# Kernel optimization log

Measured on AMD Instinct MI355X. Metric: run time of the kernel, lower is better.

Reference implementation:

```python
import jax, jax.numpy as jnp
import numpy as np

B, S, D, H, L, E, FF = 16, 1024, 384, 8, 3, 8, 768
DH = D // H
TOP_K = 2


def _ln(x, s, b):
    m = x.mean(-1, keepdims=True)
    v = x.var(-1, keepdims=True)
    return (x - m) * jax.lax.rsqrt(v + 1e-5) * s + b


def setup_inputs() -> dict:
    key = jax.random.key(0)
    ks = jax.random.split(key, 12)
    def n(k, shp, scale=0.02):
        return jax.random.normal(k, shp, jnp.float32) * scale
    return dict(
        x=jax.random.normal(ks[0], (B, S, 1), jnp.float32),
        proj_w=n(ks[1], (1, D)), proj_b=jnp.zeros((D,), jnp.float32),
        qkv_w=n(ks[2], (L, D, 3 * D)), qkv_b=jnp.zeros((L, 3 * D), jnp.float32),
        out_w=n(ks[3], (L, D, D)), out_b=jnp.zeros((L, D), jnp.float32),
        n1_s=jnp.ones((L, D), jnp.float32), n1_b=jnp.zeros((L, D), jnp.float32),
        n2_s=jnp.ones((L, D), jnp.float32), n2_b=jnp.zeros((L, D), jnp.float32),
        gate_w=n(ks[4], (L, D, E)),
        e_w1=n(ks[5], (L, E, D, FF)), e_b1=jnp.zeros((L, E, FF), jnp.float32),
        e_w2=n(ks[6], (L, E, FF, D)), e_b2=jnp.zeros((L, E, D), jnp.float32),
        att_w=n(ks[7], (D,)), att_b=jnp.zeros((), jnp.float32),
        head_w=n(ks[8], (D, 1)), head_b=jnp.zeros((1,), jnp.float32),
    )


def reference(x, proj_w, proj_b, qkv_w, qkv_b, out_w, out_b,
              n1_s, n1_b, n2_s, n2_b, gate_w, e_w1, e_b1, e_w2, e_b2,
              att_w, att_b, head_w, head_b):
    # feature projection: [B,S,1] -> [B,S,D]
    h = x @ proj_w + proj_b
    total_moe = jnp.zeros((), h.dtype)
    scale = np.float32(1.0 / np.sqrt(DH))
    for l in range(L):
        # --- pre-norm multi-head self-attention ---
        xn = _ln(h, n1_s[l], n1_b[l])
        qkv = xn @ qkv_w[l] + qkv_b[l]
        q, k, v = jnp.split(qkv, 3, axis=-1)
        q = q.reshape(B, S, H, DH)
        k = k.reshape(B, S, H, DH)
        v = v.reshape(B, S, H, DH)
        attn = jax.nn.softmax(jnp.einsum('bqhd,bkhd->bhqk', q, k) * scale, axis=-1)
        ao = jnp.einsum('bhqk,bkhd->bqhd', attn, v).reshape(B, S, D)
        h = h + (ao @ out_w[l] + out_b[l])
        # --- pre-norm top-2 gated MoE FFN ---
        xn2 = _ln(h, n2_s[l], n2_b[l])
        probs = jax.nn.softmax(xn2 @ gate_w[l], axis=-1)            # [B,S,E]
        topv, topi = jax.lax.top_k(probs, TOP_K)
        gates = topv / topv.sum(-1, keepdims=True)                  # renormalized top-2
        full = (jax.nn.one_hot(topi, E, dtype=h.dtype) * gates[..., None]).sum(-2)  # [B,S,E]
        moe_out = jnp.zeros_like(h)
        for e in range(E):  # fixed small expert loop
            ye = jax.nn.relu(xn2 @ e_w1[l, e] + e_b1[l, e]) @ e_w2[l, e] + e_b2[l, e]
            moe_out = moe_out + full[..., e:e + 1] * ye
        h = h + moe_out
        # switch-style load-balancing aux loss
        importance = probs.reshape(-1, E).mean(0)
        load = (full > 0).astype(h.dtype).reshape(-1, E).mean(0)
        total_moe = total_moe + E * jnp.sum(importance * load)
    w = jax.nn.softmax(h @ att_w + att_b, axis=1)                   # [B,S]
    pooled = jnp.einsum('bs,bsd->bd', w, h)
    rul = pooled @ head_w + head_b                                  # [B,1]
    return rul, total_moe
```

## Files before the change

### kernel.cpp

```cpp
#include <hip/hip_runtime.h>
#include <hip/hip_bf16.h>
#include <math.h>

#define TOKENS 16384
#define DMODEL 384
#define SEQ 1024
#define NHEAD 8
#define DHEAD 48
#define NEXP 8
#define FFDIM 768
#define NL 3

typedef __bf16 bf16x8 __attribute__((ext_vector_type(8)));
typedef __bf16 bf16x4 __attribute__((ext_vector_type(4)));
typedef float f32x4 __attribute__((ext_vector_type(4)));

__global__ void finalize_kernel(const int* __restrict__ counts_all,
                                const float* __restrict__ sp_all, float* __restrict__ out) {
  float tm = 0.f;
  for (int l = 0; l < NL; l++) {
    float t = 0.f;
    for (int e = 0; e < NEXP; e++)
      t += sp_all[l * NEXP + e] * (float)counts_all[l * NEXP + e];
    tm += (float)NEXP * t / ((float)TOKENS * (float)TOKENS);
  }
  out[16] = tm;
}

__global__ __launch_bounds__(256) void proj_kernel(const float* __restrict__ x,
    const float* __restrict__ pw, const float* __restrict__ pb, float* __restrict__ h) {
  int i = blockIdx.x * 256 + threadIdx.x;
  int t = i / DMODEL;
  int d = i - t * DMODEL;
  h[i] = x[t] * pw[d] + pb[d];
}

__global__ __launch_bounds__(256) void convw_kernel(const float* __restrict__ src,
    __bf16* __restrict__ dst, int K, int N) {
  __shared__ float t[32][33];
  size_t boff = (size_t)blockIdx.z * K * N;
  src += boff; dst += boff;
  int k0 = blockIdx.y * 32, n0 = blockIdx.x * 32;
  int tx = threadIdx.x & 31, ty = threadIdx.x >> 5;
#pragma unroll
  for (int i = 0; i < 32; i += 8) t[ty + i][tx] = src[(size_t)(k0 + ty + i) * N + n0 + tx];
  __syncthreads();
#pragma unroll
  for (int i = 0; i < 32; i += 8)
    dst[(size_t)(n0 + ty + i) * K + k0 + tx] = (__bf16)t[tx][ty + i];
}

__global__ __launch_bounds__(384) void ln_kernel(const float* __restrict__ src,
    __bf16* __restrict__ dst, const float* __restrict__ gs, const float* __restrict__ gb,
    int* __restrict__ zc, float* __restrict__ zs) {
  int row = blockIdx.x, tid = threadIdx.x;
  if (zc && row == 0 && tid < NEXP) { zc[tid] = 0; zs[tid] = 0.f; }
  float v = src[(size_t)row * DMODEL + tid];
  float sum = v, sq = v * v;
#pragma unroll
  for (int off = 32; off; off >>= 1) { sum += __shfl_xor(sum, off); sq += __shfl_xor(sq, off); }
  __shared__ float rs[6], rq[6];
  __shared__ float smean, sinv;
  int wid = tid >> 6;
  if ((tid & 63) == 0) { rs[wid] = sum; rq[wid] = sq; }
  __syncthreads();
  if (tid == 0) {
    float S = 0.f, Q = 0.f;
    for (int w = 0; w < 6; w++) { S += rs[w]; Q += rq[w]; }
    float mean = S / (float)DMODEL;
    float var = Q / (float)DMODEL - mean * mean;
    smean = mean; sinv = rsqrtf(var + 1e-5f);
  }
  __syncthreads();
  dst[(size_t)row * DMODEL + tid] = (__bf16)((v - smean) * sinv * gs[tid] + gb[tid]);
}

__global__ __launch_bounds__(384) void lncomb_kernel(float* __restrict__ h,
    const __bf16* __restrict__ ab, __bf16* __restrict__ dst,
    const float* __restrict__ gs, const float* __restrict__ gb) {
  int row = blockIdx.x, tid = threadIdx.x;
  size_t idx = (size_t)row * DMODEL + tid;
  float v = h[idx] + (float)ab[idx] + (float)ab[(size_t)TOKENS * DMODEL + idx];
  h[idx] = v;
  float sum = v, sq = v * v;
#pragma unroll
  for (int off = 32; off; off >>= 1) { sum += __shfl_xor(sum, off); sq += __shfl_xor(sq, off); }
  __shared__ float rs[6], rq[6];
  __shared__ float smean, sinv;
  int wid = tid >> 6;
  if ((tid & 63) == 0) { rs[wid] = sum; rq[wid] = sq; }
  __syncthreads();
  if (tid == 0) {
    float S = 0.f, Q = 0.f;
    for (int w = 0; w < 6; w++) { S += rs[w]; Q += rq[w]; }
    float mean = S / (float)DMODEL;
    float var = Q / (float)DMODEL - mean * mean;
    smean = mean; sinv = rsqrtf(var + 1e-5f);
  }
  __syncthreads();
  dst[idx] = (__bf16)((v - smean) * sinv * gs[tid] + gb[tid]);
}

template<int MODE>
__global__ __launch_bounds__(256) void mgemm_kernel(
    const __bf16* __restrict__ Abf, const __bf16* __restrict__ Wt,
    const float* __restrict__ bias, float* __restrict__ Cf, __bf16* __restrict__ Cb,
    __bf16* __restrict__ pQ, __bf16* __restrict__ pK, __bf16* __restrict__ pV,
    const int* __restrict__ counts,
    const int* __restrict__ tok_list, const float* __restrict__ gate_list,
    int N, int K) {
  int e = 0, cnt = 0, base = 0;
  const int* tl = nullptr;
  int m0 = blockIdx.y * 128;
  int n0 = blockIdx.x * 128;
  if constexpr (MODE == 2 || MODE == 3) {
    e = blockIdx.z;
    cnt = counts[e];
    if (m0 >= cnt) return;
    for (int i = 0; i < NEXP; i++) {
      int ci = counts[i];
      if (i < e) base += (ci + 63) & ~63;
    }
    tl = tok_list + e * TOKENS;
    Wt += (size_t)e * N * K;
    bias += (size_t)e * N;
  }
  __shared__ __align__(16) __bf16 smem[2][128][72];
  auto As = smem[0];
  auto Bs = smem[1];
  int tid = threadIdx.x;
  int w = tid >> 6, lane = tid & 63, c = lane & 15, g = lane >> 4;
  int arow[4], acol[4];
#pragma unroll
  for (int i = 0; i < 4; i++) {
    int chunk = tid + 256 * i;
    arow[i] = chunk >> 3;
    acol[i] = (chunk & 7) * 8;
  }
  long tok[4];
#pragma unroll
  for (int i = 0; i < 4; i++) {
    int mr = m0 + arow[i];
    if constexpr (MODE == 2)      tok[i] = (mr < cnt) ? (long)(tok_list[e * TOKENS + mr] & 0xFFFF) : -1;
    else if constexpr (MODE == 3) tok[i] = (mr < cnt) ? (long)(base + mr) : -1;
    else                          tok[i] = mr;
  }
  f32x4 acc[2][8];
#pragma unroll
  for (int m = 0; m < 2; m++)
#pragma unroll
    for (int n = 0; n < 8; n++) { acc[m][n][0] = 0.f; acc[m][n][1] = 0.f; acc[m][n][2] = 0.f; acc[m][n][3] = 0.f; }

  bf16x8 ra[4], rb[4];
  int nk = K >> 6;
#pragma unroll
  for (int i = 0; i < 4; i++) {
    bf16x8 v = {};
    if (tok[i] >= 0) v = *(const bf16x8*)&Abf[(size_t)tok[i] * K + acol[i]];
    ra[i] = v;
    rb[i] = *(const bf16x8*)&Wt[(size_t)(n0 + arow[i]) * K + acol[i]];
  }
  for (int kt = 0; kt < nk; kt++) {
#pragma unroll
    for (int i = 0; i < 4; i++) {
      *(bf16x8*)&As[arow[i]][acol[i]] = ra[i];
      *(bf16x8*)&Bs[arow[i]][acol[i]] = rb[i];
    }
    __syncthreads();
    if (kt + 1 < nk) {
      int k0 = (kt + 1) << 6;
#pragma unroll
      for (int i = 0; i < 4; i++) {
        bf16x8 v = {};
        if (tok[i] >= 0) v = *(const bf16x8*)&Abf[(size_t)tok[i] * K + k0 + acol[i]];
        ra[i] = v;
        rb[i] = *(const bf16x8*)&Wt[(size_t)(n0 + arow[i]) * K + k0 + acol[i]];
      }
    }
#pragma unroll
    for (int kk = 0; kk < 2; kk++) {
      bf16x8 a0 = *(const bf16x8*)&As[w * 32 + c][kk * 32 + g * 8];
      bf16x8 a1 = *(const bf16x8*)&As[w * 32 + 16 + c][kk * 32 + g * 8];
#pragma unroll
      for (int n = 0; n < 8; n++) {
        bf16x8 b = *(const bf16x8*)&Bs[n * 16 + c][kk * 32 + g * 8];
        acc[0][n] = __builtin_amdgcn_mfma_f32_16x16x32_bf16(a0, b, acc[0][n], 0, 0, 0);
        acc[1][n] = __builtin_amdgcn_mfma_f32_16x16x32_bf16(a1, b, acc[1][n], 0, 0, 0);
      }
    }
    __syncthreads();
  }
  if constexpr (MODE == 1) {
#pragma unroll
    for (int m = 0; m < 2; m++) {
      int row = w * 32 + m * 16 + 4 * g;
#pragma unroll
      for (int n = 0; n < 8; n++) {
        int col = n0 + n * 16 + c;
        float bv = bias[col];
#pragma unroll
        for (int r = 0; r < 4; r++)
          Cf[(size_t)(m0 + row + r) * N + col] += acc[m][n][r] + bv;
      }
    }
  } else if constexpr (MODE == 0) {
    __bf16* Ct = &smem[0][0][0];
    const int CSTR = 130;
    int which = n0 / 384;
    int rem0 = n0 - which * 384;
#pragma unroll
    for (int m = 0; m < 2; m++) {
      int row = w * 32 + m * 16 + 4 * g;
#pragma unroll
      for (int n = 0; n < 8; n++) {
        int col = n * 16 + c;
        float bv = bias[n0 + col];
#pragma unroll
        for (int r = 0; r < 4; r++) {
          float v = acc[m][n][r] + bv;
          if (which == 0) v *= 0.20823510262f;
          Ct[(row + r) * CSTR + col] = (__bf16)v;
        }
      }
    }
    __syncthreads();
    int b0 = m0 >> 10, sbase = m0 & 1023;
    if (which < 2) {
      __bf16* dstbuf = (which == 0) ? pQ : pK;
#pragma unroll
      for (int it = 0; it < 4; it++) {
        int ch = it * 256 + tid;
        int row = ch >> 3, seg = ch & 7;
        int rem = rem0 + seg * 16;
        int hd = rem / 48, d = rem - hd * 48;
        size_t bh = (size_t)(b0 * 8 + hd);
        __bf16* dst = &dstbuf[(bh * 1024 + sbase + row) * 48 + d];
        const __bf16* srcl = &Ct[row * CSTR + seg * 16];
        *(bf16x8*)&dst[0] = *(const bf16x8*)&srcl[0];
        *(bf16x8*)&dst[8] = *(const bf16x8*)&srcl[8];
      }
    } else {
      int col = tid >> 1, half = tid & 1;
      int rem = rem0 + col;
      int hd = rem / 48, d = rem - hd * 48;
      size_t bh = (size_t)(b0 * 8 + hd);
      __bf16* dst = &pV[(bh * 48 + d) * 1024 + sbase + half * 64];
      const __bf16* srcc = &Ct[(half * 64) * CSTR + col];
#pragma unroll
      for (int i8 = 0; i8 < 8; i8++) {
        bf16x8 vv;
#pragma unroll
        for (int j = 0; j < 8; j++) vv[j] = srcc[(i8 * 8 + j) * CSTR];
        *(bf16x8*)&dst[i8 * 8] = vv;
      }
    }
  } else {
    __bf16* Ct = &smem[0][0][0];
    const int CSTR = 130;
    float rowg[2][4];
    if constexpr (MODE == 3) {
#pragma unroll
      for (int m = 0; m < 2; m++)
#pragma unroll
        for (int r = 0; r < 4; r++) {
          int row = m0 + w * 32 + m * 16 + 4 * g + r;
          rowg[m][r] = (row < cnt) ? gate_list[e * TOKENS + row] : 0.f;
        }
    }
#pragma unroll
    for (int m = 0; m < 2; m++) {
      int row = w * 32 + m * 16 + 4 * g;
#pragma unroll
      for (int n = 0; n < 8; n++) {
        int col = n * 16 + c;
        float bv = bias[n0 + col];
#pragma unroll
        for (int r = 0; r < 4; r++) {
          float v = acc[m][n][r] + bv;
          if constexpr (MODE == 2) v = fmaxf(v, 0.f);
          else v *= rowg[m][r];
          Ct[(row + r) * CSTR + col] = (__bf16)v;
        }
      }
    }
    __syncthreads();
    int row = tid >> 1, half = tid & 1;
    int mr = m0 + row;
    if (mr < cnt) {
      const __bf16* srcl = &Ct[row * CSTR + half * 64];
      __bf16* dst;
      if constexpr (MODE == 2) {
        dst = &Cb[(size_t)(base + mr) * N + n0 + half * 64];
      } else {
        int entry = tl[mr];
        int t = entry & 0xFFFF, a = entry >> 16;
        dst = &Cb[((size_t)a * TOKENS + t) * DMODEL + n0 + half * 64];
      }
#pragma unroll
      for (int i = 0; i < 8; i++) *(bf16x8*)&dst[i * 8] = *(const bf16x8*)&srcl[i * 8];
    }
  }
}

__global__ __launch_bounds__(256) void combine_kernel(float* __restrict__ h,
    const __bf16* __restrict__ ab) {
  size_t i = ((size_t)blockIdx.x * 256 + threadIdx.x) * 8;
  bf16x8 a0 = *(const bf16x8*)&ab[i];
  bf16x8 a1 = *(const bf16x8*)&ab[(size_t)TOKENS * DMODEL + i];
  float* hp = h + i;
#pragma unroll
  for (int j = 0; j < 8; j++) hp[j] += (float)a0[j] + (float)a1[j];
}

__global__ __launch_bounds__(256, 4) void attn_kernel(const __bf16* __restrict__ Qh,
    const __bf16* __restrict__ Kh, const __bf16* __restrict__ VTh,
    __bf16* __restrict__ ao) {
  __shared__ __align__(16) __bf16 Ks[64][72];
  __shared__ __align__(16) __bf16 Vt[48][72];
  __shared__ __align__(16) __bf16 Ps[4][2][16][72];
  int bh = blockIdx.x;
  int q0 = blockIdx.y * 128;
  int tid = threadIdx.x;
  int w = tid >> 6, lane = tid & 63, c = lane & 15, g = lane >> 4;

  for (int i = tid; i < 192; i += 256) {
    int row = i / 3, seg = i - row * 3;
    bf16x8 z = {};
    *(bf16x8*)&Ks[row][48 + seg * 8] = z;
  }

  const __bf16* qrowA = Qh + ((size_t)bh * 1024 + q0 + w * 16 + c) * 48;
  const __bf16* qrowB = qrowA + 64 * 48;
  bf16x8 qb0a = *(const bf16x8*)&qrowA[g * 8];
  bf16x8 qb0b = *(const bf16x8*)&qrowB[g * 8];
  bf16x8 qb1a = {}, qb1b = {};
  if (g < 2) {
    qb1a = *(const bf16x8*)&qrowA[32 + g * 8];
    qb1b = *(const bf16x8*)&qrowB[32 + g * 8];
  }

  const __bf16* kb = Kh + (size_t)bh * 1024 * 48;
  const __bf16* vb = VTh + (size_t)bh * 48 * 1024;

  int r0 = tid / 6, p0 = tid - r0 * 6;
  __bf16* dst0 = &Ks[r0][p0 * 8];
  int off0 = r0 * 48 + p0 * 8;
  int e1 = tid + 256;
  __bf16* dst1; int off1; bool v1;
  if (e1 < 384) { int r = e1 / 6, p = e1 - r * 6; dst1 = &Ks[r][p * 8]; off1 = r * 48 + p * 8; v1 = false; }
  else          { int i = e1 - 384; int d = i >> 3, p = i & 7; dst1 = &Vt[d][p * 8]; off1 = d * 1024 + p * 8; v1 = true; }
  int i2 = tid + 512 - 384;
  int d2 = i2 >> 3, p2 = i2 & 7;
  __bf16* dst2 = &Vt[d2][p2 * 8];
  int off2 = d2 * 1024 + p2 * 8;

  f32x4 accA[3] = {}, accB[3] = {};
  f32x4 laccA = {}, laccB = {};
  bf16x8 ones;
#pragma unroll
  for (int j = 0; j < 8; j++) ones[j] = (__bf16)1.0f;

  for (int kt = 0; kt < 16; kt++) {
    __syncthreads();
    const __bf16* kbt = kb + (size_t)kt * 3072;
    const __bf16* vbt = vb + kt * 64;
    *(bf16x8*)dst0 = *(const bf16x8*)(kbt + off0);
    *(bf16x8*)dst1 = *(const bf16x8*)((v1 ? vbt : kbt) + off1);
    *(bf16x8*)dst2 = *(const bf16x8*)(vbt + off2);
    __syncthreads();

#pragma unroll
    for (int f = 0; f < 4; f++) {
      bf16x8 ka0 = *(const bf16x8*)&Ks[f * 16 + c][g * 8];
      bf16x8 ka1 = *(const bf16x8*)&Ks[f * 16 + c][32 + g * 8];
      f32x4 za = {}, zb = {};
      za = __builtin_amdgcn_mfma_f32_16x16x32_bf16(ka0, qb0a, za, 0, 0, 0);
      f32x4 sa = __builtin_amdgcn_mfma_f32_16x16x32_bf16(ka1, qb1a, za, 0, 0, 0);
      zb = __builtin_amdgcn_mfma_f32_16x16x32_bf16(ka0, qb0b, zb, 0, 0, 0);
      f32x4 sb = __builtin_amdgcn_mfma_f32_16x16x32_bf16(ka1, qb1b, zb, 0, 0, 0);
      bf16x4 pka = { (__bf16)__builtin_amdgcn_exp2f(sa[0]), (__bf16)__builtin_amdgcn_exp2f(sa[1]),
                     (__bf16)__builtin_amdgcn_exp2f(sa[2]), (__bf16)__builtin_amdgcn_exp2f(sa[3]) };
      bf16x4 pkb = { (__bf16)__builtin_amdgcn_exp2f(sb[0]), (__bf16)__builtin_amdgcn_exp2f(sb[1]),
                     (__bf16)__builtin_amdgcn_exp2f(sb[2]), (__bf16)__builtin_amdgcn_exp2f(sb[3]) };
      *(bf16x4*)&Ps[w][0][c][f * 16 + 4 * g] = pka;
      *(bf16x4*)&Ps[w][1][c][f * 16 + 4 * g] = pkb;
    }
    bf16x8 pa0a = *(const bf16x8*)&Ps[w][0][c][g * 8];
    bf16x8 pa1a = *(const bf16x8*)&Ps[w][0][c][32 + g * 8];
    bf16x8 pa0b = *(const bf16x8*)&Ps[w][1][c][g * 8];
    bf16x8 pa1b = *(const bf16x8*)&Ps[w][1][c][32 + g * 8];
#pragma unroll
    for (int t = 0; t < 3; t++) {
      bf16x8 vb0 = *(const bf16x8*)&Vt[t * 16 + c][g * 8];
      bf16x8 vb1 = *(const bf16x8*)&Vt[t * 16 + c][32 + g * 8];
      accA[t] = __builtin_amdgcn_mfma_f32_16x16x32_bf16(pa0a, vb0, accA[t], 0, 0, 0);
      accA[t] = __builtin_amdgcn_mfma_f32_16x16x32_bf16(pa1a, vb1, accA[t], 0, 0, 0);
      accB[t] = __builtin_amdgcn_mfma_f32_16x16x32_bf16(pa0b, vb0, accB[t], 0, 0, 0);
      accB[t] = __builtin_amdgcn_mfma_f32_16x16x32_bf16(pa1b, vb1, accB[t], 0, 0, 0);
    }
    laccA = __builtin_amdgcn_mfma_f32_16x16x32_bf16(pa0a, ones, laccA, 0, 0, 0);
    laccA = __builtin_amdgcn_mfma_f32_16x16x32_bf16(pa1a, ones, laccA, 0, 0, 0);
    laccB = __builtin_amdgcn_mfma_f32_16x16x32_bf16(pa0b, ones, laccB, 0, 0, 0);
    laccB = __builtin_amdgcn_mfma_f32_16x16x32_bf16(pa1b, ones, laccB, 0, 0, 0);
  }
  float linvA[4], linvB[4];
#pragma unroll
  for (int r = 0; r < 4; r++) { linvA[r] = 1.f / laccA[r]; linvB[r] = 1.f / laccB[r]; }
  int b = bh >> 3, hh = bh & 7;
#pragma unroll
  for (int t = 0; t < 3; t++)
#pragma unroll
    for (int r = 0; r < 4; r++) {
      size_t rowA = (size_t)(b * SEQ + q0 + w * 16 + 4 * g + r);
      ao[rowA * DMODEL + hh * 48 + t * 16 + c] = (__bf16)(accA[t][r] * linvA[r]);
      ao[(rowA + 64) * DMODEL + hh * 48 + t * 16 + c] = (__bf16)(accB[t][r] * linvB[r]);
    }
}

__global__ __launch_bounds__(256) void gate_kernel(const __bf16* __restrict__ xnb,
    const float* __restrict__ gw, int* __restrict__ counts, float* __restrict__ sum_probs,
    int* __restrict__ tok_list, float* __restrict__ gate_list) {
  __shared__ float Gs[NEXP][DMODEL];
  __shared__ float simp[NEXP];
  __shared__ int hist[NEXP], basep[NEXP];
  __shared__ unsigned char tokE[32][2];
  __shared__ float tokG[32][2];
  __shared__ short rankS[32][2];
  int tid = threadIdx.x;
  for (int i = tid; i < DMODEL * NEXP; i += 256) {
    int d = i >> 3, e2 = i & 7;
    Gs[e2][d] = gw[i];
  }
  if (tid < NEXP) { simp[tid] = 0.f; hist[tid] = 0; }
  __syncthreads();
  int w = tid >> 6, lane = tid & 63;
  int tbase = blockIdx.x * 32 + w * 8;
  float impacc[NEXP] = {};
  for (int tt = 0; tt < 8; tt++) {
    int t = tbase + tt;
    float p[NEXP] = {};
#pragma unroll
    for (int j = 0; j < 6; j++) {
      int d = lane + 64 * j;
      float xv = (float)xnb[(size_t)t * DMODEL + d];
#pragma unroll
      for (int e2 = 0; e2 < NEXP; e2++) p[e2] += xv * Gs[e2][d];
    }
#pragma unroll
    for (int off = 32; off; off >>= 1)
#pragma unroll
      for (int e2 = 0; e2 < NEXP; e2++) p[e2] += __shfl_xor(p[e2], off);
    float mx = p[0];
#pragma unroll
    for (int e2 = 1; e2 < NEXP; e2++) mx = fmaxf(mx, p[e2]);
    float s = 0.f;
#pragma unroll
    for (int e2 = 0; e2 < NEXP; e2++) { p[e2] = __expf(p[e2] - mx); s += p[e2]; }
    float inv = 1.f / s;
#pragma unroll
    for (int e2 = 0; e2 < NEXP; e2++) { p[e2] *= inv; impacc[e2] += p[e2]; }
    int i0 = 0; float v0 = p[0];
#pragma unroll
    for (int e2 = 1; e2 < NEXP; e2++) if (p[e2] > v0) { v0 = p[e2]; i0 = e2; }
    int i1 = -1; float v1 = -INFINITY;
#pragma unroll
    for (int e2 = 0; e2 < NEXP; e2++) if (e2 != i0 && p[e2] > v1) { v1 = p[e2]; i1 = e2; }
    if (lane == 0) {
      float gsum = v0 + v1;
      int r0 = atomicAdd(&hist[i0], 1);
      int r1 = atomicAdd(&hist[i1], 1);
      int sl = w * 8 + tt;
      tokE[sl][0] = (unsigned char)i0; tokE[sl][1] = (unsigned char)i1;
      tokG[sl][0] = v0 / gsum;         tokG[sl][1] = v1 / gsum;
      rankS[sl][0] = (short)r0;        rankS[sl][1] = (short)r1;
    }
  }
  if (lane == 0)
#pragma unroll
    for (int e2 = 0; e2 < NEXP; e2++) atomicAdd(&simp[e2], impacc[e2]);
  __syncthreads();
  if (tid < NEXP) {
    basep[tid] = atomicAdd(&counts[tid], hist[tid]);
    atomicAdd(&sum_probs[tid], simp[tid]);
  }
  __syncthreads();
  int t0 = blockIdx.x * 32;
  if (tid < 64) {
    int sl = tid >> 1, a = tid & 1;
    int e2 = tokE[sl][a];
    int pos = basep[e2] + rankS[sl][a];
    tok_list[e2 * TOKENS + pos] = (t0 + sl) | (a << 16);
    gate_list[e2 * TOKENS + pos] = tokG[sl][a];
  }
}

__global__ __launch_bounds__(256) void head1_kernel(const float* __restrict__ h,
    const float* __restrict__ att_w, const float* __restrict__ att_b,
    float* __restrict__ logits) {
  int tid = threadIdx.x;
  int w = tid >> 6, lane = tid & 63;
  float4 aw0 = *(const float4*)&att_w[lane * 4];
  float2 aw1 = *(const float2*)&att_w[256 + lane * 2];
  float ab = att_b[0];
  for (int i = w; i < 32; i += 4) {
    int t = blockIdx.x * 32 + i;
    const float* hr = h + (size_t)t * DMODEL;
    float4 v4 = *(const float4*)&hr[lane * 4];
    float2 v2 = *(const float2*)&hr[256 + lane * 2];
    float dot = v4.x * aw0.x + v4.y * aw0.y + v4.z * aw0.z + v4.w * aw0.w
              + v2.x * aw1.x + v2.y * aw1.y;
#pragma unroll
    for (int off = 32; off; off >>= 1) dot += __shfl_xor(dot, off);
    if (lane == 0) logits[t] = dot + ab;
  }
}

__global__ __launch_bounds__(256) void head2_kernel(float* __restrict__ logits) {
  int b = blockIdx.x, tid = threadIdx.x;
  int w = tid >> 6, lane = tid & 63;
  float* lb = logits + b * SEQ;
  __shared__ float red[4];
  float lv[4];
  float mx = -INFINITY;
#pragma unroll
  for (int i = 0; i < 4; i++) { lv[i] = lb[tid + 256 * i]; mx = fmaxf(mx, lv[i]); }
#pragma unroll
  for (int off = 32; off; off >>= 1) mx = fmaxf(mx, __shfl_xor(mx, off));
  if (lane == 0) red[w] = mx;
  __syncthreads();
  mx = fmaxf(fmaxf(red[0], red[1]), fmaxf(red[2], red[3]));
  __syncthreads();
  float s = 0.f;
#pragma unroll
  for (int i = 0; i < 4; i++) { lv[i] = __expf(lv[i] - mx); s += lv[i]; }
#pragma unroll
  for (int off = 32; off; off >>= 1) s += __shfl_xor(s, off);
  if (lane == 0) red[w] = s;
  __syncthreads();
  float inv = 1.f / (red[0] + red[1] + red[2] + red[3]);
#pragma unroll
  for (int i = 0; i < 4; i++) lb[tid + 256 * i] = lv[i] * inv;
}

__global__ __launch_bounds__(256) void head3a_kernel(const float* __restrict__ h,
    const float* __restrict__ wnorm, float* __restrict__ partial) {
  int b = blockIdx.x, dc = blockIdx.y, sc = blockIdx.z;
  int tid = threadIdx.x;
  int d = tid & 63, sg = tid >> 6;
  const float* hb = h + (size_t)b * SEQ * DMODEL + dc * 64 + d;
  const float* wb = wnorm + b * SEQ + sc * 64;
  float acc = 0.f;
  int s0 = sc * 64 + sg * 16;
#pragma unroll
  for (int i = 0; i < 16; i++)
    acc += wb[sg * 16 + i] * hb[(size_t)(s0 + i) * DMODEL];
  __shared__ float red[256];
  red[tid] = acc;
  __syncthreads();
  if (sg == 0)
    partial[(((size_t)b * 6 + dc) * 16 + sc) * 64 + d] =
        red[d] + red[64 + d] + red[128 + d] + red[192 + d];
}

__global__ void head3b_kernel(const float* __restrict__ partial,
    const float* __restrict__ head_w, float* __restrict__ part) {
  int b = blockIdx.x, dc = blockIdx.y;
  int d = threadIdx.x;
  const float* pp = partial + (((size_t)b * 6 + dc) * 16) * 64 + d;
  float pooled = 0.f;
#pragma unroll
  for (int sc = 0; sc < 16; sc++) pooled += pp[sc * 64];
  float pd = pooled * head_w[dc * 64 + d];
#pragma unroll
  for (int off = 32; off; off >>= 1) pd += __shfl_xor(pd, off);
  if (d == 0) part[b * 6 + dc] = pd;
}

__global__ void head4_kernel(const float* __restrict__ part,
                             const float* __restrict__ head_b, float* __restrict__ out) {
  int b = threadIdx.x;
  if (b < 16) {
    float s = head_b[0];
#pragma unroll
    for (int dc = 0; dc < 6; dc++) s += part[b * 6 + dc];
    out[b] = s;
  }
}

extern "C" void kernel_launch(void* const* d_in, const int* in_sizes, int n_in,
                              void* d_out, int out_size, void* d_ws, size_t ws_size,
                              hipStream_t stream) {
  (void)in_sizes; (void)n_in; (void)out_size; (void)ws_size;
  const float* x      = (const float*)d_in[0];
  const float* proj_w = (const float*)d_in[1];
  const float* proj_b = (const float*)d_in[2];
  const float* qkv_w  = (const float*)d_in[3];
  const float* qkv_b  = (const float*)d_in[4];
  const float* out_w  = (const float*)d_in[5];
  const float* out_b  = (const float*)d_in[6];
  const float* n1_s   = (const float*)d_in[7];
  const float* n1_b   = (const float*)d_in[8];
  const float* n2_s   = (const float*)d_in[9];
  const float* n2_b   = (const float*)d_in[10];
  const float* gate_w = (const float*)d_in[11];
  const float* e_w1   = (const float*)d_in[12];
  const float* e_b1   = (const float*)d_in[13];
  const float* e_w2   = (const float*)d_in[14];
  const float* e_b2   = (const float*)d_in[15];
  const float* att_w  = (const float*)d_in[16];
  const float* att_b  = (const float*)d_in[17];
  const float* head_w = (const float*)d_in[18];
  const float* head_b = (const float*)d_in[19];
  float* out = (float*)d_out;

  char* wsb = (char*)d_ws;
  float*  h    = (float*)(wsb);
  __bf16* xnb  = (__bf16*)(wsb + 25165824);
  __bf16* aob  = (__bf16*)(wsb + 37748736);
  __bf16* ab   = (__bf16*)(wsb + 25165824);
  __bf16* uni  = (__bf16*)(wsb + 50331648);
  __bf16* Qh   = uni;
  __bf16* Khd  = (__bf16*)(wsb + 62914560);
  __bf16* VTh  = (__bf16*)(wsb + 75497472);
  __bf16* qkvWt = (__bf16*)(wsb + 101449728);
  __bf16* outWt = (__bf16*)(wsb + 104103936);
  __bf16* e1Wt  = (__bf16*)(wsb + 104988672);
  __bf16* e2Wt  = (__bf16*)(wsb + 119144448);
  char* sm = wsb + 133300224;
  int*   counts_all = (int*)(sm);
  float* sp_all     = (float*)(sm + 128);
  int*   tok_list  = (int*)(sm + 256);
  float* gate_list = (float*)(sm + 256 + 524288);
  float* logits    = (float*)(sm + 1048832);
  float* part      = (float*)(sm + 1048832 + 65536);
  float* partial   = (float*)(sm + 1048832 + 131072);

  convw_kernel<<<dim3(36, 12, 3), 256, 0, stream>>>(qkv_w, qkvWt, 384, 1152);
  convw_kernel<<<dim3(12, 12, 3), 256, 0, stream>>>(out_w, outWt, 384, 384);
  convw_kernel<<<dim3(24, 12, 24), 256, 0, stream>>>(e_w1, e1Wt, 384, 768);
  convw_kernel<<<dim3(12, 24, 24), 256, 0, stream>>>(e_w2, e2Wt, 768, 384);

  proj_kernel<<<TOKENS * DMODEL / 256, 256, 0, stream>>>(x, proj_w, proj_b, h);
  ln_kernel<<<TOKENS, 384, 0, stream>>>(h, xnb, n1_s, n1_b, nullptr, nullptr);

  for (int l = 0; l < NL; l++) {
    int*   counts = counts_all + l * NEXP;
    float* sp     = sp_all + l * NEXP;
    mgemm_kernel<0><<<dim3(9, 128), 256, 0, stream>>>(
        xnb, qkvWt + (size_t)l * 1152 * 384, qkv_b + l * 1152, nullptr, nullptr,
        Qh, Khd, VTh, nullptr, nullptr, nullptr, 1152, 384);
    attn_kernel<<<dim3(128, 8), 256, 0, stream>>>(Qh, Khd, VTh, aob);
    mgemm_kernel<1><<<dim3(3, 128), 256, 0, stream>>>(
        aob, outWt + (size_t)l * 384 * 384, out_b + l * 384, h, nullptr,
        nullptr, nullptr, nullptr, nullptr, nullptr, nullptr, 384, 384);
    ln_kernel<<<TOKENS, 384, 0, stream>>>(h, xnb, n2_s + l * DMODEL, n2_b + l * DMODEL,
                                          counts, sp);
    gate_kernel<<<512, 256, 0, stream>>>(xnb, gate_w + (size_t)l * DMODEL * NEXP,
                                         counts, sp, tok_list, gate_list);
    mgemm_kernel<2><<<dim3(6, 128, 8), 256, 0, stream>>>(
        xnb, e1Wt + (size_t)l * 8 * 768 * 384, e_b1 + l * 8 * FFDIM, nullptr, uni,
        nullptr, nullptr, nullptr, counts, tok_list, nullptr, 768, 384);
    mgemm_kernel<3><<<dim3(3, 128, 8), 256, 0, stream>>>(
        uni, e2Wt + (size_t)l * 8 * 384 * 768, e_b2 + l * 8 * DMODEL, nullptr, ab,
        nullptr, nullptr, nullptr, counts, tok_list, gate_list, 384, 768);
    if (l + 1 < NL) {
      lncomb_kernel<<<TOKENS, 384, 0, stream>>>(h, ab, xnb,
          n1_s + (l + 1) * DMODEL, n1_b + (l + 1) * DMODEL);
    } else {
      combine_kernel<<<TOKENS * DMODEL / (256 * 8), 256, 0, stream>>>(h, ab);
    }
  }

  head1_kernel<<<512, 256, 0, stream>>>(h, att_w, att_b, logits);
  head2_kernel<<<16, 256, 0, stream>>>(logits);
  head3a_kernel<<<dim3(16, 6, 16), 256, 0, stream>>>(h, logits, partial);
  head3b_kernel<<<dim3(16, 6), 64, 0, stream>>>(partial, head_w, part);
  head4_kernel<<<1, 64, 0, stream>>>(part, head_b, out);
  finalize_kernel<<<1, 1, 0, stream>>>(counts_all, sp_all, out);
}
```

Before: 886.3 us.

## Load GEMM A operand directly from global into MFMA fragments, bypassing LDS

The GEMM kernel no longer stages the A tile (activations or gathered tokens) through shared memory. Each lane loads its MFMA A fragments straight from global memory, and only the weight tile goes through LDS. Shared memory is shrunk to a single buffer sized for the epilogue. This removes half the LDS traffic and allows higher occupancy, but each wave now issues uncoalesced 16-byte row loads, and the A loads are issued after the MFMAs, so their latency is less hidden.

```diff
diff --git a/kernel.cpp b/kernel.cpp
--- a/kernel.cpp
+++ b/kernel.cpp
@@ -125,9 +125,8 @@
     Wt += (size_t)e * N * K;
     bias += (size_t)e * N;
   }
-  __shared__ __align__(16) __bf16 smem[2][128][72];
-  auto As = smem[0];
-  auto Bs = smem[1];
+  __shared__ __align__(16) __bf16 smem[128][130];
+  auto Bs = reinterpret_cast<__bf16(*)[72]>(&smem[0][0]);
   int tid = threadIdx.x;
   int w = tid >> 6, lane = tid & 63, c = lane & 15, g = lane >> 4;
   int arow[4], acol[4];
@@ -137,13 +136,19 @@
     arow[i] = chunk >> 3;
     acol[i] = (chunk & 7) * 8;
   }
-  long tok[4];
-#pragma unroll
-  for (int i = 0; i < 4; i++) {
-    int mr = m0 + arow[i];
-    if constexpr (MODE == 2)      tok[i] = (mr < cnt) ? (long)(tok_list[e * TOKENS + mr] & 0xFFFF) : -1;
-    else if constexpr (MODE == 3) tok[i] = (mr < cnt) ? (long)(base + mr) : -1;
-    else                          tok[i] = mr;
+  int r1 = w * 32 + c, r2 = r1 + 16;
+  long tokf0, tokf1;
+  {
+    int mr1 = m0 + r1, mr2 = m0 + r2;
+    if constexpr (MODE == 2) {
+      tokf0 = (mr1 < cnt) ? (long)(tl[mr1] & 0xFFFF) : -1;
+      tokf1 = (mr2 < cnt) ? (long)(tl[mr2] & 0xFFFF) : -1;
+    } else if constexpr (MODE == 3) {
+      tokf0 = (mr1 < cnt) ? (long)(base + mr1) : -1;
+      tokf1 = (mr2 < cnt) ? (long)(base + mr2) : -1;
+    } else {
+      tokf0 = mr1; tokf1 = mr2;
+    }
   }
   f32x4 acc[2][8];
 #pragma unroll
@@ -151,41 +156,51 @@
 #pragma unroll
     for (int n = 0; n < 8; n++) { acc[m][n][0] = 0.f; acc[m][n][1] = 0.f; acc[m][n][2] = 0.f; acc[m][n][3] = 0.f; }
 
-  bf16x8 ra[4], rb[4];
+  bf16x8 rb[4];
+  bf16x8 af0a = {}, af0b = {}, af1a = {}, af1b = {};
   int nk = K >> 6;
 #pragma unroll
-  for (int i = 0; i < 4; i++) {
-    bf16x8 v = {};
-    if (tok[i] >= 0) v = *(const bf16x8*)&Abf[(size_t)tok[i] * K + acol[i]];
-    ra[i] = v;
+  for (int i = 0; i < 4; i++)
     rb[i] = *(const bf16x8*)&Wt[(size_t)(n0 + arow[i]) * K + acol[i]];
+  if (tokf0 >= 0) {
+    af0a = *(const bf16x8*)&Abf[(size_t)tokf0 * K + g * 8];
+    af0b = *(const bf16x8*)&Abf[(size_t)tokf0 * K + 32 + g * 8];
+  }
+  if (tokf1 >= 0) {
+    af1a = *(const bf16x8*)&Abf[(size_t)tokf1 * K + g * 8];
+    af1b = *(const bf16x8*)&Abf[(size_t)tokf1 * K + 32 + g * 8];
   }
   for (int kt = 0; kt < nk; kt++) {
 #pragma unroll
-    for (int i = 0; i < 4; i++) {
-      *(bf16x8*)&As[arow[i]][acol[i]] = ra[i];
+    for (int i = 0; i < 4; i++)
       *(bf16x8*)&Bs[arow[i]][acol[i]] = rb[i];
-    }
     __syncthreads();
+    int k0 = (kt + 1) << 6;
     if (kt + 1 < nk) {
-      int k0 = (kt + 1) << 6;
-#pragma unroll
-      for (int i = 0; i < 4; i++) {
-        bf16x8 v = {};
-        if (tok[i] >= 0) v = *(const bf16x8*)&Abf[(size_t)tok[i] * K + k0 + acol[i]];
-        ra[i] = v;
+#pragma unroll
+      for (int i = 0; i < 4; i++)
         rb[i] = *(const bf16x8*)&Wt[(size_t)(n0 + arow[i]) * K + k0 + acol[i]];
-      }
-    }
-#pragma unroll
-    for (int kk = 0; kk < 2; kk++) {
-      bf16x8 a0 = *(const bf16x8*)&As[w * 32 + c][kk * 32 + g * 8];
-      bf16x8 a1 = *(const bf16x8*)&As[w * 32 + 16 + c][kk * 32 + g * 8];
-#pragma unroll
-      for (int n = 0; n < 8; n++) {
-        bf16x8 b = *(const bf16x8*)&Bs[n * 16 + c][kk * 32 + g * 8];
-        acc[0][n] = __builtin_amdgcn_mfma_f32_16x16x32_bf16(a0, b, acc[0][n], 0, 0, 0);
-        acc[1][n] = __builtin_amdgcn_mfma_f32_16x16x32_bf16(a1, b, acc[1][n], 0, 0, 0);
+    }
+#pragma unroll
+    for (int n = 0; n < 8; n++) {
+      bf16x8 b0 = *(const bf16x8*)&Bs[n * 16 + c][g * 8];
+      acc[0][n] = __builtin_amdgcn_mfma_f32_16x16x32_bf16(af0a, b0, acc[0][n], 0, 0, 0);
+      acc[1][n] = __builtin_amdgcn_mfma_f32_16x16x32_bf16(af1a, b0, acc[1][n], 0, 0, 0);
+    }
+#pragma unroll
+    for (int n = 0; n < 8; n++) {
+      bf16x8 b1 = *(const bf16x8*)&Bs[n * 16 + c][32 + g * 8];
+      acc[0][n] = __builtin_amdgcn_mfma_f32_16x16x32_bf16(af0b, b1, acc[0][n], 0, 0, 0);
+      acc[1][n] = __builtin_amdgcn_mfma_f32_16x16x32_bf16(af1b, b1, acc[1][n], 0, 0, 0);
+    }
+    if (kt + 1 < nk) {
+      if (tokf0 >= 0) {
+        af0a = *(const bf16x8*)&Abf[(size_t)tokf0 * K + k0 + g * 8];
+        af0b = *(const bf16x8*)&Abf[(size_t)tokf0 * K + k0 + 32 + g * 8];
+      }
+      if (tokf1 >= 0) {
+        af1a = *(const bf16x8*)&Abf[(size_t)tokf1 * K + k0 + g * 8];
+        af1b = *(const bf16x8*)&Abf[(size_t)tokf1 * K + k0 + 32 + g * 8];
       }
     }
     __syncthreads();
@@ -204,7 +219,7 @@
       }
     }
   } else if constexpr (MODE == 0) {
-    __bf16* Ct = &smem[0][0][0];
+    __bf16* Ct = &smem[0][0];
     const int CSTR = 130;
     int which = n0 / 384;
     int rem0 = n0 - which * 384;
@@ -255,7 +270,7 @@
       }
     }
   } else {
-    __bf16* Ct = &smem[0][0][0];
+    __bf16* Ct = &smem[0][0];
     const int CSTR = 130;
     float rowg[2][4];
     if constexpr (MODE == 3) {
```

After: 873.6 us. About the same (-1.4%).
